# Kernel optimization log

Measured on AMD Instinct MI355X. Metric: run time of the kernel, lower is better.

The kernel has to match this reference:

```python
import jax, jax.numpy as jnp
import numpy as np

EPS = 1e-12

def l2_normalize(x, axis=-1):
    # matches torch F.normalize(p=2, dim=1, eps=1e-12) for 2D input
    n = jnp.sqrt(jnp.sum(x * x, axis=axis, keepdims=True))
    return x / jnp.maximum(n, EPS)

def setup_inputs() -> dict:
    key = jax.random.key(0)
    ks = jax.random.split(key, 7)
    N, D = 8192, 256
    s = 1.0 / np.sqrt(D)
    x = jax.random.normal(ks[0], (N, D), dtype=jnp.float32)
    Wq = jax.random.uniform(ks[1], (D, D), jnp.float32, -s, s)
    bq = jax.random.uniform(ks[2], (D,), jnp.float32, -s, s)
    Wk = jax.random.uniform(ks[3], (D, D), jnp.float32, -s, s)
    bk = jax.random.uniform(ks[4], (D,), jnp.float32, -s, s)
    Wv = jax.random.uniform(ks[5], (D, D), jnp.float32, -s, s)
    bv = jax.random.uniform(ks[6], (D,), jnp.float32, -s, s)
    return {"x": x, "Wq": Wq, "bq": bq, "Wk": Wk, "bk": bk, "Wv": Wv, "bv": bv}

def reference(x, Wq, bq, Wk, bk, Wv, bv):
    q = l2_normalize(x @ Wq.T + bq)           # [N, D]
    k = l2_normalize(x @ Wk.T + bk)           # [N, D]
    v = x @ Wv.T + bv                         # [N, D]
    cos_sim = q @ k.T                         # [N, N]
    w = jax.nn.relu(cos_sim)
    # zero diagonal, then renormalize rows to sum 1
    N = w.shape[0]
    w = jnp.where(jnp.eye(N, dtype=bool), 0.0, w)
    w = w / jnp.maximum(jnp.sum(w, axis=-1, keepdims=True), EPS)
    return w @ v + x
```

## Files before the change

### kernel.cpp

```cpp
#include <hip/hip_runtime.h>

#define NROWS 8192
#define DDIM  256
#define KSPLIT 4
#define BM 128
#define BK 64
#define NT (NROWS / KSPLIT / BK)

typedef __bf16 bf16x8 __attribute__((ext_vector_type(8)));
typedef float  f32x4  __attribute__((ext_vector_type(4)));
typedef float  f32x16 __attribute__((ext_vector_type(16)));

typedef __attribute__((address_space(1))) unsigned int uint_gas;
typedef __attribute__((address_space(3))) unsigned int uint_las;

__device__ __forceinline__ void gload_lds16(const void* g, void* l) {
  __builtin_amdgcn_global_load_lds((const uint_gas*)g, (uint_las*)l, 16, 0, 0);
}

__device__ __forceinline__ unsigned int f2bf_bits(float f) {
  union { float f; unsigned int u; } v; v.f = f;
  unsigned int r = v.u + 0x7FFFu + ((v.u >> 16) & 1u);
  return r >> 16;
}
__device__ __forceinline__ float bf2f(unsigned int b) {
  union { unsigned int u; float f; } v; v.u = b << 16;
  return v.f;
}
__device__ __forceinline__ unsigned int pack2bf(float a, float b) {
  union { unsigned int u; __bf16 h[2]; } p;
  p.h[0] = (__bf16)a; p.h[1] = (__bf16)b;
  return p.u;
}
__device__ __forceinline__ unsigned short f2h_bits(float f) {
  union { _Float16 h; unsigned short u; } c; c.h = (_Float16)f;
  return c.u;
}
__device__ __forceinline__ float h2f(unsigned short u) {
  union { unsigned short u; _Float16 h; } c; c.u = u;
  return (float)c.h;
}

#define NXFRAG (512 * 8 * 64)
#define NWFRAG (3 * 16 * 8 * 64)
__global__ __launch_bounds__(256) void convert_kernel(
    const float* __restrict__ x, const float* __restrict__ wq,
    const float* __restrict__ wk, const float* __restrict__ wv,
    unsigned short* __restrict__ xp, unsigned short* __restrict__ Wp)
{
  int tid = blockIdx.x * 256 + threadIdx.x;
  const float* src;
  unsigned short* dst;
  int row, col;
  if (tid < NXFRAG) {
    int l = tid & 63, ks = (tid >> 6) & 7, rt = tid >> 9;
    src = x; dst = xp + (size_t)tid * 8;
    row = rt * 16 + (l & 15); col = ks * 32 + (l >> 4) * 8;
  } else {
    int fid = tid - NXFRAG;
    if (fid >= NWFRAG) return;
    int l = fid & 63, ks = (fid >> 6) & 7, ct = (fid >> 9) & 15, out = fid >> 13;
    src = (out == 0) ? wq : (out == 1) ? wk : wv;
    dst = Wp + (size_t)fid * 8;
    row = ct * 16 + (l & 15); col = ks * 32 + (l >> 4) * 8;
  }
  const float* p = src + (size_t)row * DDIM + col;
  float4 f0 = *(const float4*)p;
  float4 f1 = *(const float4*)(p + 4);
  ushort4 o0, o1;
  o0.x = (unsigned short)f2bf_bits(f0.x); o0.y = (unsigned short)f2bf_bits(f0.y);
  o0.z = (unsigned short)f2bf_bits(f0.z); o0.w = (unsigned short)f2bf_bits(f0.w);
  o1.x = (unsigned short)f2bf_bits(f1.x); o1.y = (unsigned short)f2bf_bits(f1.y);
  o1.z = (unsigned short)f2bf_bits(f1.z); o1.w = (unsigned short)f2bf_bits(f1.w);
  *(ushort4*)dst = o0;
  *(ushort4*)(dst + 4) = o1;
}

__global__ __launch_bounds__(256) void qkv_kernel(
    const float* __restrict__ bq, const float* __restrict__ bk, const float* __restrict__ bv,
    const unsigned short* __restrict__ xp, const unsigned short* __restrict__ Wp,
    unsigned short* __restrict__ qb, unsigned short* __restrict__ kb,
    unsigned short* __restrict__ vtp)
{
  __shared__ unsigned short vstage[DDIM * 72];
  const int t = threadIdx.x;
  const int w = t >> 6, l = t & 63;
  const int c = l & 15, g = l >> 4;
  const int out = blockIdx.x / 128;
  const int mb  = blockIdx.x % 128;
  const int row0 = mb * 64;
  const int rw = row0 + w * 16;
  const int rt = mb * 4 + w;

  bf16x8 a[8];
  #pragma unroll
  for (int ks = 0; ks < 8; ks++)
    a[ks] = *(const bf16x8*)(xp + ((size_t)(rt * 8 + ks) * 64 + l) * 8);

  const float* bias = (out == 0) ? bq : (out == 1) ? bk : bv;
  f32x4 vals[16];
  #pragma unroll
  for (int ct = 0; ct < 16; ct++) {
    f32x4 acc = {0.f, 0.f, 0.f, 0.f};
    #pragma unroll
    for (int ks = 0; ks < 8; ks++) {
      bf16x8 b = *(const bf16x8*)(Wp + ((size_t)((out * 16 + ct) * 8 + ks) * 64 + l) * 8);
      acc = __builtin_amdgcn_mfma_f32_16x16x32_bf16(a[ks], b, acc, 0, 0, 0);
    }
    float bias_v = bias[ct * 16 + c];
    #pragma unroll
    for (int r = 0; r < 4; r++) acc[r] += bias_v;
    vals[ct] = acc;
  }
  if (out < 2) {
    #pragma unroll
    for (int r = 0; r < 4; r++) {
      float ss = 0.f;
      #pragma unroll
      for (int ct = 0; ct < 16; ct++) ss += vals[ct][r] * vals[ct][r];
      ss += __shfl_xor(ss, 1); ss += __shfl_xor(ss, 2);
      ss += __shfl_xor(ss, 4); ss += __shfl_xor(ss, 8);
      float inv = 1.f / fmaxf(sqrtf(ss), 1e-12f);
      #pragma unroll
      for (int ct = 0; ct < 16; ct++) vals[ct][r] *= inv;
    }
    unsigned short* dst = (out == 0) ? qb : kb;
    #pragma unroll
    for (int ct = 0; ct < 16; ct++) {
      #pragma unroll
      for (int r = 0; r < 4; r++) {
        unsigned int bits = f2bf_bits(vals[ct][r]);
        unsigned int ob = (unsigned int)__shfl_xor((int)bits, 1);
        if (!(l & 1))
          *(unsigned int*)(dst + (size_t)(rw + g * 4 + r) * DDIM + ct * 16 + c) =
              bits | (ob << 16);
      }
    }
  } else {
    #pragma unroll
    for (int ct = 0; ct < 16; ct++)
      #pragma unroll
      for (int r = 0; r < 4; r++)
        vstage[(ct * 16 + c) * 72 + (w * 16 + g * 4 + r)] =
            (unsigned short)f2bf_bits(vals[ct][r]);
    __syncthreads();
    unsigned short* wdst = vtp + (size_t)mb * 16384;
    #pragma unroll
    for (int p = 0; p < 8; p++) {
      int n = p * 256 + t;
      int dg = ((n >> 8) << 5) + (n & 31);
      int s  = (n >> 5) & 7;
      *(uint4*)(wdst + (size_t)n * 8) = *(const uint4*)(vstage + dg * 72 + s * 8);
    }
  }
}

__global__ __launch_bounds__(1024, 4) void attn_kernel(
    const unsigned short* __restrict__ qb, const unsigned short* __restrict__ kb,
    const unsigned short* __restrict__ vtp,
    unsigned short* __restrict__ nump, float* __restrict__ denp)
{
  __shared__ __align__(16) char smem[98304];
  char* kbuf = smem;
  char* Pb   = smem + 65536;

  const int t = threadIdx.x;
  const int w = t >> 6, l = t & 63;
  const int l31 = l & 31, hi = l >> 5;
  const int rw = w & 7;
  const int ts = t & 511;
  const int bid = blockIdx.x;
  const int split = bid & (KSPLIT - 1);
  const int mb = bid >> 2;
  const int q0 = mb * BM;
  const int kbase0 = split * (NROWS / KSPLIT);
  const char* kbc = (const char*)kb;
  const char* vtc = (const char*)vtp;

  if (w < 8) {
    const int sr = rw >> 1, sc = rw & 1;
    const int qrow = sr * 32 + l31;
    const int qrowg = q0 + qrow;
    const int krl = sc * 32 + l31;

    bf16x8 qa[16];
    {
      const unsigned short* qrowp = qb + (size_t)(q0 + qrow) * DDIM + hi * 8;
      #pragma unroll
      for (int m = 0; m < 16; m++) qa[m] = *(const bf16x8*)(qrowp + m * 16);
    }
    float denl = 0.f;

    auto stageK = [&](int buf, int it) {
      const char* ksrc = kbc + (size_t)(kbase0 + it * BK) * 512;
      #pragma unroll
      for (int i = 0; i < 4; i++) {
        int n = i * 512 + ts;
        int row = n >> 5, slot = n & 31;
        gload_lds16(ksrc + row * 512 + (((slot - row) & 31) << 4),
                    kbuf + buf * 32768 + i * 8192 + rw * 1024);
      }
    };

    stageK(0, 0);
    asm volatile("s_waitcnt vmcnt(0)" ::: "memory");
    __builtin_amdgcn_sched_barrier(0);
    __builtin_amdgcn_s_barrier();
    __builtin_amdgcn_sched_barrier(0);

    for (int it = 0; it < NT; ++it) {
      const int cur = it & 1;
      if (it + 1 < NT) stageK(cur ^ 1, it + 1);
      __builtin_amdgcn_sched_barrier(0);

      const char* kcur = kbuf + cur * 32768;
      f32x16 sacc = (f32x16){0.f};
      #pragma unroll
      for (int m = 0; m < 16; m++) {
        bf16x8 kf = *(const bf16x8*)(kcur + krl * 512 +
                                     (((m * 2 + hi + krl) & 31) << 4));
        sacc = __builtin_amdgcn_mfma_f32_32x32x16_bf16(kf, qa[m], sacc, 0, 0, 0);
      }
      char* pbase = Pb + cur * 16384 + sr * 4096 + l31 * 16 + hi * 8;
      const int kbase = kbase0 + it * BK;
      if (__builtin_expect(kbase < q0 + BM && q0 < kbase + BK, 0)) {
        const int dref = qrowg - (kbase + sc * 32 + hi * 4);
        #pragma unroll
        for (int q = 0; q < 4; q++) {
          float v0 = fmaxf(sacc[4 * q + 0], 0.f);
          float v1 = fmaxf(sacc[4 * q + 1], 0.f);
          float v2 = fmaxf(sacc[4 * q + 2], 0.f);
          float v3 = fmaxf(sacc[4 * q + 3], 0.f);
          const int d = dref - 8 * q;
          v0 = (d == 0) ? 0.f : v0;
          v1 = (d == 1) ? 0.f : v1;
          v2 = (d == 2) ? 0.f : v2;
          v3 = (d == 3) ? 0.f : v3;
          denl += (v0 + v1) + (v2 + v3);
          uint2 d2;
          d2.x = pack2bf(v0, v1);
          d2.y = pack2bf(v2, v3);
          *(uint2*)(pbase + (sc * 4 + q) * 512) = d2;
        }
      } else {
        #pragma unroll
        for (int q = 0; q < 4; q++) {
          float v0 = fmaxf(sacc[4 * q + 0], 0.f);
          float v1 = fmaxf(sacc[4 * q + 1], 0.f);
          float v2 = fmaxf(sacc[4 * q + 2], 0.f);
          float v3 = fmaxf(sacc[4 * q + 3], 0.f);
          denl += (v0 + v1) + (v2 + v3);
          uint2 d2;
          d2.x = pack2bf(v0, v1);
          d2.y = pack2bf(v2, v3);
          *(uint2*)(pbase + (sc * 4 + q) * 512) = d2;
        }
      }
      asm volatile("s_waitcnt vmcnt(0) lgkmcnt(0)" ::: "memory");
      __builtin_amdgcn_sched_barrier(0);
      __builtin_amdgcn_s_barrier();
      __builtin_amdgcn_sched_barrier(0);
    }

    float d = denl;
    d += __shfl_xor(d, 32);
    if (l < 32)
      denp[((size_t)split * 2 + sc) * NROWS + q0 + sr * 32 + l] = d;
  } else {
    const int pr = rw >> 2, pc = rw & 3;

    f32x16 oacc[2][2];
    #pragma unroll
    for (int rt = 0; rt < 2; rt++)
      #pragma unroll
      for (int dt = 0; dt < 2; dt++)
        oacc[rt][dt] = (f32x16){0.f};

    bf16x8 vfrA[8], vfrB[8];

    auto loadV = [&](bf16x8 (&dst)[8], int it) {
      const char* vsrc = vtc + (size_t)((kbase0 + it * BK) >> 6) * 32768;
      #pragma unroll
      for (int ch = 0; ch < 4; ch++)
        #pragma unroll
        for (int dt = 0; dt < 2; dt++)
          dst[ch * 2 + dt] = *(const bf16x8*)(vsrc + (pc * 2 + dt) * 4096 +
                                              (ch * 2 + hi) * 512 + l31 * 16);
    };
    auto pvcomp = [&](const bf16x8 (&vfr)[8], const char* Pprev) {
      #pragma unroll
      for (int ch = 0; ch < 4; ch++) {
        const int s512 = (ch * 2 + hi) * 512 + l31 * 16;
        bf16x8 pa0 = *(const bf16x8*)(Pprev + (pr * 2 + 0) * 4096 + s512);
        bf16x8 pa1 = *(const bf16x8*)(Pprev + (pr * 2 + 1) * 4096 + s512);
        #pragma unroll
        for (int dt = 0; dt < 2; dt++) {
          oacc[0][dt] = __builtin_amdgcn_mfma_f32_32x32x16_bf16(pa0, vfr[ch * 2 + dt],
                                                                oacc[0][dt], 0, 0, 0);
          oacc[1][dt] = __builtin_amdgcn_mfma_f32_32x32x16_bf16(pa1, vfr[ch * 2 + dt],
                                                                oacc[1][dt], 0, 0, 0);
        }
      }
    };

    __builtin_amdgcn_s_barrier();
    __builtin_amdgcn_sched_barrier(0);

    for (int it2 = 0; it2 < NT; it2 += 2) {
      loadV(vfrA, it2);
      if (it2 > 0) pvcomp(vfrB, Pb + 16384);
      asm volatile("s_waitcnt lgkmcnt(0)" ::: "memory");
      __builtin_amdgcn_sched_barrier(0);
      __builtin_amdgcn_s_barrier();
      __builtin_amdgcn_sched_barrier(0);
      loadV(vfrB, it2 + 1);
      pvcomp(vfrA, Pb + 0);
      asm volatile("s_waitcnt lgkmcnt(0)" ::: "memory");
      __builtin_amdgcn_sched_barrier(0);
      __builtin_amdgcn_s_barrier();
      __builtin_amdgcn_sched_barrier(0);
    }
    pvcomp(vfrB, Pb + 16384);

    unsigned short* np = nump + (size_t)split * NROWS * DDIM;
    #pragma unroll
    for (int rt = 0; rt < 2; rt++)
      #pragma unroll
      for (int dt = 0; dt < 2; dt++)
        #pragma unroll
        for (int r = 0; r < 16; r++) {
          int rowg = q0 + pr * 64 + rt * 32 + (r & 3) + 8 * (r >> 2) + 4 * hi;
          int col  = pc * 64 + dt * 32 + l31;
          np[(size_t)rowg * DDIM + col] = f2h_bits(oacc[rt][dt][r]);
        }
  }
}

__global__ __launch_bounds__(256) void combine_kernel(
    const float* __restrict__ x,
    const unsigned short* __restrict__ nump, const float* __restrict__ denp,
    float* __restrict__ out)
{
  const int t = threadIdx.x;
  const int w = t >> 6, l = t & 63;
  const int i = blockIdx.x * 4 + w;

  float den = 0.f;
  #pragma unroll
  for (int sp = 0; sp < KSPLIT * 2; sp++)
    den += denp[(size_t)sp * NROWS + i];
  float inv = 1.f / fmaxf(den, 1e-12f);

  const int d0 = l * 4;
  float4 acc = {0.f, 0.f, 0.f, 0.f};
  #pragma unroll
  for (int sp = 0; sp < KSPLIT; sp++) {
    ushort4 u4 = *(const ushort4*)(nump + ((size_t)sp * NROWS + i) * DDIM + d0);
    acc.x += h2f(u4.x); acc.y += h2f(u4.y);
    acc.z += h2f(u4.z); acc.w += h2f(u4.w);
  }
  float4 xx = *(const float4*)(x + (size_t)i * DDIM + d0);
  float4 o;
  o.x = acc.x * inv + xx.x;
  o.y = acc.y * inv + xx.y;
  o.z = acc.z * inv + xx.z;
  o.w = acc.w * inv + xx.w;
  *(float4*)(out + (size_t)i * DDIM + d0) = o;
}

extern "C" void kernel_launch(void* const* d_in, const int* in_sizes, int n_in,
                              void* d_out, int out_size, void* d_ws, size_t ws_size,
                              hipStream_t stream)
{
  const float* x  = (const float*)d_in[0];
  const float* Wq = (const float*)d_in[1];
  const float* bq = (const float*)d_in[2];
  const float* Wk = (const float*)d_in[3];
  const float* bk = (const float*)d_in[4];
  const float* Wv = (const float*)d_in[5];
  const float* bv = (const float*)d_in[6];

  char* ws = (char*)d_ws;
  unsigned short* xp   = (unsigned short*)(ws + 0);
  unsigned short* Wp   = (unsigned short*)(ws + 4194304);
  unsigned short* qb   = (unsigned short*)(ws + 4587520);
  unsigned short* kb   = (unsigned short*)(ws + 8781824);
  unsigned short* vtp  = (unsigned short*)(ws + 12976128);
  unsigned short* nump = (unsigned short*)(ws + 17170432);
  float* denp = (float*)(ws + 33947648);

  convert_kernel<<<1120, 256, 0, stream>>>(x, Wq, Wk, Wv, xp, Wp);
  qkv_kernel<<<384, 256, 0, stream>>>(bq, bk, bv, xp, Wp, qb, kb, vtp);
  attn_kernel<<<(NROWS / BM) * KSPLIT, 1024, 0, stream>>>(qb, kb, vtp, nump, denp);
  combine_kernel<<<NROWS / 4, 256, 0, stream>>>(x, nump, denp, (float*)d_out);
}
```

Baseline: 122.2 us.

## Fuse x bf16 conversion into QKV kernel, split S accumulators, raise MFMA priority

The bf16 conversion of x moves out of the separate convert kernel and into the QKV projection kernel, which now reads fp32 x directly. This removes the 4 MB xp write and read, and the convert launch shrinks to the weights only. The attention score loop now uses two independent accumulators to break the MFMA dependency chain, and both MFMA phases are wrapped in s_setprio. In exchange, each QKV block reads fp32 x (twice the bytes), and x is re-read by all three projection blocks.

```diff
diff --git a/kernel.cpp b/kernel.cpp
--- a/kernel.cpp
+++ b/kernel.cpp
@@ -40,30 +40,32 @@
   union { unsigned short u; _Float16 h; } c; c.u = u;
   return (float)c.h;
 }
-
-#define NXFRAG (512 * 8 * 64)
+__device__ __forceinline__ bf16x8 cvt8(const float* p) {
+  float4 f0 = *(const float4*)p;
+  float4 f1 = *(const float4*)(p + 4);
+  union { bf16x8 v; unsigned short s[8]; } u;
+  u.s[0] = (unsigned short)f2bf_bits(f0.x);
+  u.s[1] = (unsigned short)f2bf_bits(f0.y);
+  u.s[2] = (unsigned short)f2bf_bits(f0.z);
+  u.s[3] = (unsigned short)f2bf_bits(f0.w);
+  u.s[4] = (unsigned short)f2bf_bits(f1.x);
+  u.s[5] = (unsigned short)f2bf_bits(f1.y);
+  u.s[6] = (unsigned short)f2bf_bits(f1.z);
+  u.s[7] = (unsigned short)f2bf_bits(f1.w);
+  return u.v;
+}
+
 #define NWFRAG (3 * 16 * 8 * 64)
 __global__ __launch_bounds__(256) void convert_kernel(
-    const float* __restrict__ x, const float* __restrict__ wq,
-    const float* __restrict__ wk, const float* __restrict__ wv,
-    unsigned short* __restrict__ xp, unsigned short* __restrict__ Wp)
+    const float* __restrict__ wq, const float* __restrict__ wk,
+    const float* __restrict__ wv, unsigned short* __restrict__ Wp)
 {
-  int tid = blockIdx.x * 256 + threadIdx.x;
-  const float* src;
-  unsigned short* dst;
-  int row, col;
-  if (tid < NXFRAG) {
-    int l = tid & 63, ks = (tid >> 6) & 7, rt = tid >> 9;
-    src = x; dst = xp + (size_t)tid * 8;
-    row = rt * 16 + (l & 15); col = ks * 32 + (l >> 4) * 8;
-  } else {
-    int fid = tid - NXFRAG;
-    if (fid >= NWFRAG) return;
-    int l = fid & 63, ks = (fid >> 6) & 7, ct = (fid >> 9) & 15, out = fid >> 13;
-    src = (out == 0) ? wq : (out == 1) ? wk : wv;
-    dst = Wp + (size_t)fid * 8;
-    row = ct * 16 + (l & 15); col = ks * 32 + (l >> 4) * 8;
-  }
+  int fid = blockIdx.x * 256 + threadIdx.x;
+  if (fid >= NWFRAG) return;
+  int l = fid & 63, ks = (fid >> 6) & 7, ct = (fid >> 9) & 15, out = fid >> 13;
+  const float* src = (out == 0) ? wq : (out == 1) ? wk : wv;
+  unsigned short* dst = Wp + (size_t)fid * 8;
+  int row = ct * 16 + (l & 15), col = ks * 32 + (l >> 4) * 8;
   const float* p = src + (size_t)row * DDIM + col;
   float4 f0 = *(const float4*)p;
   float4 f1 = *(const float4*)(p + 4);
@@ -78,7 +80,7 @@
 
 __global__ __launch_bounds__(256) void qkv_kernel(
     const float* __restrict__ bq, const float* __restrict__ bk, const float* __restrict__ bv,
-    const unsigned short* __restrict__ xp, const unsigned short* __restrict__ Wp,
+    const float* __restrict__ x, const unsigned short* __restrict__ Wp,
     unsigned short* __restrict__ qb, unsigned short* __restrict__ kb,
     unsigned short* __restrict__ vtp)
 {
@@ -90,12 +92,11 @@
   const int mb  = blockIdx.x % 128;
   const int row0 = mb * 64;
   const int rw = row0 + w * 16;
-  const int rt = mb * 4 + w;
 
   bf16x8 a[8];
   #pragma unroll
   for (int ks = 0; ks < 8; ks++)
-    a[ks] = *(const bf16x8*)(xp + ((size_t)(rt * 8 + ks) * 64 + l) * 8);
+    a[ks] = cvt8(x + (size_t)(rw + c) * DDIM + ks * 32 + g * 8);
 
   const float* bias = (out == 0) ? bq : (out == 1) ? bk : bv;
   f32x4 vals[16];
@@ -214,23 +215,29 @@
       __builtin_amdgcn_sched_barrier(0);
 
       const char* kcur = kbuf + cur * 32768;
-      f32x16 sacc = (f32x16){0.f};
-      #pragma unroll
-      for (int m = 0; m < 16; m++) {
-        bf16x8 kf = *(const bf16x8*)(kcur + krl * 512 +
-                                     (((m * 2 + hi + krl) & 31) << 4));
-        sacc = __builtin_amdgcn_mfma_f32_32x32x16_bf16(kf, qa[m], sacc, 0, 0, 0);
+      f32x16 sacc0 = (f32x16){0.f};
+      f32x16 sacc1 = (f32x16){0.f};
+      __builtin_amdgcn_s_setprio(1);
+      #pragma unroll
+      for (int m = 0; m < 8; m++) {
+        bf16x8 kf0 = *(const bf16x8*)(kcur + krl * 512 +
+                                      ((((2 * m) * 2 + hi + krl) & 31) << 4));
+        bf16x8 kf1 = *(const bf16x8*)(kcur + krl * 512 +
+                                      ((((2 * m + 1) * 2 + hi + krl) & 31) << 4));
+        sacc0 = __builtin_amdgcn_mfma_f32_32x32x16_bf16(kf0, qa[2 * m], sacc0, 0, 0, 0);
+        sacc1 = __builtin_amdgcn_mfma_f32_32x32x16_bf16(kf1, qa[2 * m + 1], sacc1, 0, 0, 0);
       }
+      __builtin_amdgcn_s_setprio(0);
       char* pbase = Pb + cur * 16384 + sr * 4096 + l31 * 16 + hi * 8;
       const int kbase = kbase0 + it * BK;
       if (__builtin_expect(kbase < q0 + BM && q0 < kbase + BK, 0)) {
         const int dref = qrowg - (kbase + sc * 32 + hi * 4);
         #pragma unroll
         for (int q = 0; q < 4; q++) {
-          float v0 = fmaxf(sacc[4 * q + 0], 0.f);
-          float v1 = fmaxf(sacc[4 * q + 1], 0.f);
-          float v2 = fmaxf(sacc[4 * q + 2], 0.f);
-          float v3 = fmaxf(sacc[4 * q + 3], 0.f);
+          float v0 = fmaxf(sacc0[4 * q + 0] + sacc1[4 * q + 0], 0.f);
+          float v1 = fmaxf(sacc0[4 * q + 1] + sacc1[4 * q + 1], 0.f);
+          float v2 = fmaxf(sacc0[4 * q + 2] + sacc1[4 * q + 2], 0.f);
+          float v3 = fmaxf(sacc0[4 * q + 3] + sacc1[4 * q + 3], 0.f);
           const int d = dref - 8 * q;
           v0 = (d == 0) ? 0.f : v0;
           v1 = (d == 1) ? 0.f : v1;
@@ -245,10 +252,10 @@
       } else {
         #pragma unroll
         for (int q = 0; q < 4; q++) {
-          float v0 = fmaxf(sacc[4 * q + 0], 0.f);
-          float v1 = fmaxf(sacc[4 * q + 1], 0.f);
-          float v2 = fmaxf(sacc[4 * q + 2], 0.f);
-          float v3 = fmaxf(sacc[4 * q + 3], 0.f);
+          float v0 = fmaxf(sacc0[4 * q + 0] + sacc1[4 * q + 0], 0.f);
+          float v1 = fmaxf(sacc0[4 * q + 1] + sacc1[4 * q + 1], 0.f);
+          float v2 = fmaxf(sacc0[4 * q + 2] + sacc1[4 * q + 2], 0.f);
+          float v3 = fmaxf(sacc0[4 * q + 3] + sacc1[4 * q + 3], 0.f);
           denl += (v0 + v1) + (v2 + v3);
           uint2 d2;
           d2.x = pack2bf(v0, v1);
@@ -288,6 +295,7 @@
                                               (ch * 2 + hi) * 512 + l31 * 16);
     };
     auto pvcomp = [&](const bf16x8 (&vfr)[8], const char* Pprev) {
+      __builtin_amdgcn_s_setprio(1);
       #pragma unroll
       for (int ch = 0; ch < 4; ch++) {
         const int s512 = (ch * 2 + hi) * 512 + l31 * 16;
@@ -301,6 +309,7 @@
                                                                 oacc[1][dt], 0, 0, 0);
         }
       }
+      __builtin_amdgcn_s_setprio(0);
     };
 
     __builtin_amdgcn_s_barrier();
@@ -381,16 +390,15 @@
   const float* bv = (const float*)d_in[6];
 
   char* ws = (char*)d_ws;
-  unsigned short* xp   = (unsigned short*)(ws + 0);
-  unsigned short* Wp   = (unsigned short*)(ws + 4194304);
-  unsigned short* qb   = (unsigned short*)(ws + 4587520);
-  unsigned short* kb   = (unsigned short*)(ws + 8781824);
-  unsigned short* vtp  = (unsigned short*)(ws + 12976128);
-  unsigned short* nump = (unsigned short*)(ws + 17170432);
-  float* denp = (float*)(ws + 33947648);
-
-  convert_kernel<<<1120, 256, 0, stream>>>(x, Wq, Wk, Wv, xp, Wp);
-  qkv_kernel<<<384, 256, 0, stream>>>(bq, bk, bv, xp, Wp, qb, kb, vtp);
+  unsigned short* Wp   = (unsigned short*)(ws + 0);
+  unsigned short* qb   = (unsigned short*)(ws + 393216);
+  unsigned short* kb   = (unsigned short*)(ws + 4587520);
+  unsigned short* vtp  = (unsigned short*)(ws + 8781824);
+  unsigned short* nump = (unsigned short*)(ws + 12976128);
+  float* denp = (float*)(ws + 29753344);
+
+  convert_kernel<<<96, 256, 0, stream>>>(Wq, Wk, Wv, Wp);
+  qkv_kernel<<<384, 256, 0, stream>>>(bq, bk, bv, x, Wp, qb, kb, vtp);
   attn_kernel<<<(NROWS / BM) * KSPLIT, 1024, 0, stream>>>(qb, kb, vtp, nump, denp);
   combine_kernel<<<NROWS / 4, 256, 0, stream>>>(x, nump, denp, (float*)d_out);
 }
```

Result: slower. 147.9 us (+21.0%).
